# Optimization experiments

Measured on AMD Instinct MI355X. Metric: run time of the kernel, lower is better.

## Reference

```python
import jax, jax.numpy as jnp
import numpy as np

NEG_SLOPE = 0.2
LN_EPS = 1e-5


def setup_inputs() -> dict:
    key = jax.random.key(0)
    k1, k2, k3, k4 = jax.random.split(key, 4)
    B, K, D, H = 64, 256, 1024, 2
    x = jax.random.normal(k1, (B, K, D), dtype=jnp.float32)
    adj = jax.random.randint(k2, (K, K), 0, 2, dtype=jnp.int32)
    # Xavier-ish scaling for weights
    W = jax.random.normal(k3, (D, D), dtype=jnp.float32) * (1.0 / np.sqrt(D))
    a = jax.random.normal(k4, (H, 2 * D), dtype=jnp.float32) * (1.0 / np.sqrt(2 * D))
    gamma = jnp.ones((D,), dtype=jnp.float32)
    beta = jnp.zeros((D,), dtype=jnp.float32)
    return {"x": x, "adj": adj, "W": W, "a": a, "gamma": gamma, "beta": beta}


def _layer_norm(y, gamma, beta):
    mu = jnp.mean(y, axis=-1, keepdims=True)
    var = jnp.mean(jnp.square(y - mu), axis=-1, keepdims=True)
    return (y - mu) * jax.lax.rsqrt(var + LN_EPS) * gamma + beta


def reference(x, adj, W, a, gamma, beta):
    # x: (B,K,D), adj: (K,K), W: (D,D), a: (H,2D)
    D = W.shape[1]
    h = jnp.einsum("bki,io->bko", x, W)  # (B,K,D)
    # GAT trick: a^T [h_i; h_j] = a_src . h_i + a_dst . h_j (same math as
    # the huge pairwise-concat + Linear in the original module).
    a_src, a_dst = a[:, :D], a[:, D:]  # each (H,D)
    f_i = jnp.einsum("bkd,hd->bhk", h, a_src)  # (B,H,K)
    f_j = jnp.einsum("bkd,hd->bhk", h, a_dst)  # (B,H,K)
    e = f_i[:, :, :, None] + f_j[:, :, None, :]  # (B,H,K,K)
    e = jnp.where(e >= 0, e, NEG_SLOPE * e)  # LeakyReLU
    mask = (adj != 0)[None, None]  # (1,1,K,K)
    e = jnp.where(mask, e, -jnp.inf)
    attn = jax.nn.softmax(e, axis=-1)
    attn = jnp.where(jnp.isnan(attn), 0.0, attn)  # nan_to_num for all-masked rows
    # dropout is identity in eval mode
    head_out = jnp.einsum("bhij,bjd->bhid", attn, h)  # (B,H,K,D)
    out = jnp.mean(head_out, axis=1)  # average heads, (B,K,D)
    out = _layer_norm(out + x, gamma, beta)  # residual is Identity (in_dim==out_dim)
    return out
```

## Files before the change

### kernel.cpp

```cpp
#include <hip/hip_runtime.h>
#include <hip/hip_bf16.h>

#define KN 256
#define DD 1024
#define HH 2

typedef __attribute__((ext_vector_type(8))) short short8;
typedef __attribute__((ext_vector_type(4))) float f32x4;

__device__ __forceinline__ ushort f2b(float f) {
  union { float f; unsigned u; } v; v.f = f;
  unsigned u = v.u;
  return (ushort)((u + 0x7fffu + ((u >> 16) & 1u)) >> 16);
}
__device__ __forceinline__ float b2f(ushort h) {
  union { unsigned u; float f; } v; v.u = ((unsigned)h) << 16;
  return v.f;
}
__device__ __forceinline__ void gload16(const ushort* g, ushort* l) {
  __builtin_amdgcn_global_load_lds(
      (const __attribute__((address_space(1))) void*)g,
      (__attribute__((address_space(3))) void*)l, 16, 0, 0);
}

__global__ __launch_bounds__(256) void k_conv(const float* __restrict__ x,
                                              ushort* __restrict__ xb) {
  int c0 = blockIdx.x * 256 + threadIdx.x;
  for (int it = 0; it < 4; ++it) {
    size_t i = ((size_t)c0 + (size_t)it * 524288) * 8;
    float4 v0 = *reinterpret_cast<const float4*>(&x[i]);
    float4 v1 = *reinterpret_cast<const float4*>(&x[i + 4]);
    short8 o;
    o[0] = (short)f2b(v0.x); o[1] = (short)f2b(v0.y);
    o[2] = (short)f2b(v0.z); o[3] = (short)f2b(v0.w);
    o[4] = (short)f2b(v1.x); o[5] = (short)f2b(v1.y);
    o[6] = (short)f2b(v1.z); o[7] = (short)f2b(v1.w);
    *reinterpret_cast<short8*>(&xb[i]) = o;
  }
}

__global__ __launch_bounds__(256) void k_wT(const float* __restrict__ W, ushort* __restrict__ WTb) {
  __shared__ float t[32][33];
  int tx = threadIdx.x, ty = threadIdx.y;
  int x = blockIdx.x * 32 + tx;
  int y0 = blockIdx.y * 32 + ty;
  for (int i = 0; i < 32; i += 8)
    t[ty + i][tx] = W[(size_t)(y0 + i) * DD + x];
  __syncthreads();
  int xo = blockIdx.y * 32 + tx;
  int yo = blockIdx.x * 32 + ty;
  for (int i = 0; i < 32; i += 8)
    WTb[(size_t)(yo + i) * DD + xo] = f2b(t[tx][ty + i]);
}

__global__ __launch_bounds__(512, 2) void k_gemm_h(const ushort* __restrict__ xb,
                                                   const ushort* __restrict__ WTb,
                                                   ushort* __restrict__ hT) {
  __shared__ ushort As[2][16384];
  __shared__ ushort Bs[2][16384];
  const int tid = threadIdx.x;
  const int w = tid >> 6, lane = tid & 63;
  const int bn = blockIdx.x;
  const int b  = blockIdx.y;
  const int wm = (w >> 2) * 128, wn = (w & 3) * 64;
  const int r16 = lane & 15, kqi = lane >> 4;
  const ushort* gA0 = xb + (size_t)(b * 256) * DD;
  const ushort* gB0 = WTb + (size_t)(bn * 256) * DD;
  const int srow0 = tid >> 3;
  const int scc   = (tid & 7) ^ ((tid >> 3) & 7);
  const int sdst0 = (tid & ~63) * 8;
  const int cs0 = (kqi)     ^ (r16 & 7);
  const int cs1 = (kqi + 4) ^ (r16 & 7);
  f32x4 acc[8][4] = {};
  short8 bfv[4][2];

#define STG(ISB, BUF, H, KB)                                                    \
  {                                                                             \
    const ushort* g0_ = (ISB) ? gB0 : gA0;                                      \
    ushort* l0_ = (ISB) ? Bs[BUF] : As[BUF];                                    \
    gload16(g0_ + (size_t)((H) * 128 + srow0) * DD + (KB) + scc * 8,            \
            l0_ + (H) * 8192 + sdst0);                                          \
    gload16(g0_ + (size_t)((H) * 128 + 64 + srow0) * DD + (KB) + scc * 8,       \
            l0_ + (H) * 8192 + 4096 + sdst0);                                   \
  }

#define PHASE(Q, BUF, LOADB, WMODE, STAGE_STMT)                                 \
  {                                                                             \
    short8 af0[2], af1[2];                                                      \
    {                                                                           \
      const ushort* Ab_ = As[BUF];                                              \
      int ra_ = (wm + (Q) * 32 + r16) * 64;                                     \
      int rb_ = (wm + (Q) * 32 + 16 + r16) * 64;                                \
      af0[0] = *(const short8*)(Ab_ + ra_ + cs0 * 8);                           \
      af0[1] = *(const short8*)(Ab_ + ra_ + cs1 * 8);                           \
      af1[0] = *(const short8*)(Ab_ + rb_ + cs0 * 8);                           \
      af1[1] = *(const short8*)(Ab_ + rb_ + cs1 * 8);                           \
    }                                                                           \
    if (LOADB) {                                                                \
      const ushort* Bb_ = Bs[BUF];                                              \
      _Pragma("unroll")                                                         \
      for (int nf = 0; nf < 4; ++nf) {                                          \
        int rn_ = (wn + nf * 16 + r16) * 64;                                    \
        bfv[nf][0] = *(const short8*)(Bb_ + rn_ + cs0 * 8);                     \
        bfv[nf][1] = *(const short8*)(Bb_ + rn_ + cs1 * 8);                     \
      }                                                                         \
    }                                                                           \
    STAGE_STMT;                                                                 \
    __builtin_amdgcn_s_barrier();                                               \
    asm volatile("s_waitcnt lgkmcnt(0)" ::: "memory");                          \
    __builtin_amdgcn_sched_barrier(0);                                          \
    __builtin_amdgcn_s_setprio(1);                                              \
    _Pragma("unroll")                                                           \
    for (int nf = 0; nf < 4; ++nf) {                                            \
      acc[(Q)*2][nf]   = __builtin_amdgcn_mfma_f32_16x16x32_bf16(af0[0], bfv[nf][0], acc[(Q)*2][nf], 0, 0, 0);     \
      acc[(Q)*2+1][nf] = __builtin_amdgcn_mfma_f32_16x16x32_bf16(af1[0], bfv[nf][0], acc[(Q)*2+1][nf], 0, 0, 0);   \
    }                                                                           \
    _Pragma("unroll")                                                           \
    for (int nf = 0; nf < 4; ++nf) {                                            \
      acc[(Q)*2][nf]   = __builtin_amdgcn_mfma_f32_16x16x32_bf16(af0[1], bfv[nf][1], acc[(Q)*2][nf], 0, 0, 0);     \
      acc[(Q)*2+1][nf] = __builtin_amdgcn_mfma_f32_16x16x32_bf16(af1[1], bfv[nf][1], acc[(Q)*2+1][nf], 0, 0, 0);   \
    }                                                                           \
    __builtin_amdgcn_s_setprio(0);                                              \
    __builtin_amdgcn_sched_barrier(0);                                          \
    if ((WMODE) == 1) { asm volatile("s_waitcnt vmcnt(6)" ::: "memory"); }      \
    else if ((WMODE) == 2) { asm volatile("s_waitcnt vmcnt(0)" ::: "memory"); } \
    __builtin_amdgcn_s_barrier();                                               \
  }

  STG(1, 0, 0, 0) STG(1, 0, 1, 0) STG(0, 0, 0, 0) STG(0, 0, 1, 0)
  STG(1, 1, 0, 64) STG(1, 1, 1, 64) STG(0, 1, 0, 64)
  asm volatile("s_waitcnt vmcnt(6)" ::: "memory");
  __builtin_amdgcn_sched_barrier(0);
  __builtin_amdgcn_s_barrier();

  for (int i = 0; i < 8; ++i) {
    const int k1 = i * 128 + 64;
    const int k2 = i * 128 + 128;
    const int k3 = i * 128 + 192;
    const bool s2 = (k2 < 1024), s3 = (k3 < 1024);
    const int wt = (i < 7) ? 1 : 2;
    PHASE(0, 0, 1, 0,  { STG(0, 1, 1, k1) })
    PHASE(1, 0, 0, 0,  { if (s2) STG(1, 0, 0, k2) })
    PHASE(2, 0, 0, 0,  { if (s2) STG(1, 0, 1, k2) })
    PHASE(3, 0, 0, wt, { if (s2) STG(0, 0, 0, k2) })
    PHASE(0, 1, 1, 0,  { if (s2) STG(0, 0, 1, k2) })
    PHASE(1, 1, 0, 0,  { if (s3) STG(1, 1, 0, k3) })
    PHASE(2, 1, 0, 0,  { if (s3) STG(1, 1, 1, k3) })
    PHASE(3, 1, 0, wt, { if (s3) STG(0, 1, 0, k3) })
  }
#undef PHASE
#undef STG

  const int g = lane >> 4;
  #pragma unroll
  for (int mf = 0; mf < 8; ++mf) {
    int j0 = wm + mf * 16 + g * 4;
    #pragma unroll
    for (int nf = 0; nf < 4; ++nf) {
      int C = bn * 256 + wn + nf * 16 + r16;
      ushort4 o;
      o.x = f2b(acc[mf][nf][0]); o.y = f2b(acc[mf][nf][1]);
      o.z = f2b(acc[mf][nf][2]); o.w = f2b(acc[mf][nf][3]);
      *reinterpret_cast<ushort4*>(&hT[((size_t)b * DD + C) * KN + j0]) = o;
    }
  }
}

__global__ __launch_bounds__(256) void k_f(const ushort* __restrict__ hT,
                                           const float* __restrict__ a,
                                           float* __restrict__ fip, float* __restrict__ fjp) {
  __shared__ float als[4][256];
  int b = blockIdx.x, dq = blockIdx.y;
  int tid = threadIdx.x;
  for (int v = 0; v < 4; ++v) als[v][tid] = a[v * DD + dq * 256 + tid];
  __syncthreads();
  const ushort* base = hT + ((size_t)b * DD + dq * 256) * KN + tid;
  float a0 = 0.f, a1 = 0.f, a2 = 0.f, a3 = 0.f;
  #pragma unroll 8
  for (int d = 0; d < 256; ++d) {
    float hv = b2f(base[(size_t)d * KN]);
    a0 += hv * als[0][d];
    a1 += hv * als[1][d];
    a2 += hv * als[2][d];
    a3 += hv * als[3][d];
  }
  size_t o = ((size_t)(dq * 64 + b) * HH) * KN + tid;
  fip[o] = a0;
  fjp[o] = a1;
  fip[o + KN] = a2;
  fjp[o + KN] = a3;
}

__global__ __launch_bounds__(256) void k_attn(const float* __restrict__ fip, const float* __restrict__ fjp,
                                              const int* __restrict__ adj, ushort* __restrict__ Pb) {
  int w = threadIdx.x >> 6, l = threadIdx.x & 63;
  int gw = blockIdx.x * 4 + w;
  int b = gw >> 8, i = gw & 255;
  int4 am = *reinterpret_cast<const int4*>(adj + i * KN + l * 4);
  int msk[4] = { am.x, am.y, am.z, am.w };
  float fi0 = 0.f, fi1 = 0.f;
  float fj0[4] = {0.f, 0.f, 0.f, 0.f}, fj1[4] = {0.f, 0.f, 0.f, 0.f};
  for (int dq = 0; dq < 4; ++dq) {
    size_t o = ((size_t)(dq * 64 + b) * HH) * KN;
    fi0 += fip[o + i];
    fi1 += fip[o + KN + i];
    float4 t0 = *reinterpret_cast<const float4*>(&fjp[o + l * 4]);
    float4 t1 = *reinterpret_cast<const float4*>(&fjp[o + KN + l * 4]);
    fj0[0] += t0.x; fj0[1] += t0.y; fj0[2] += t0.z; fj0[3] += t0.w;
    fj1[0] += t1.x; fj1[1] += t1.y; fj1[2] += t1.z; fj1[3] += t1.w;
  }
  float e0[4], e1[4];
  const float NEGINF = -3.0e38f;
  float m0 = NEGINF, m1 = NEGINF;
  for (int e = 0; e < 4; ++e) {
    float v0 = fi0 + fj0[e], v1 = fi1 + fj1[e];
    v0 = v0 >= 0.f ? v0 : 0.2f * v0;
    v1 = v1 >= 0.f ? v1 : 0.2f * v1;
    e0[e] = v0; e1[e] = v1;
    if (msk[e]) { m0 = fmaxf(m0, v0); m1 = fmaxf(m1, v1); }
  }
  for (int off = 1; off < 64; off <<= 1) {
    m0 = fmaxf(m0, __shfl_xor(m0, off));
    m1 = fmaxf(m1, __shfl_xor(m1, off));
  }
  float p0[4], p1[4], s0 = 0.f, s1 = 0.f;
  for (int e = 0; e < 4; ++e) {
    p0[e] = msk[e] ? __expf(e0[e] - m0) : 0.f;
    p1[e] = msk[e] ? __expf(e1[e] - m1) : 0.f;
    s0 += p0[e]; s1 += p1[e];
  }
  for (int off = 1; off < 64; off <<= 1) {
    s0 += __shfl_xor(s0, off);
    s1 += __shfl_xor(s1, off);
  }
  float i0 = s0 > 0.f ? 1.f / s0 : 0.f;
  float i1 = s1 > 0.f ? 1.f / s1 : 0.f;
  ushort4 o;
  o.x = f2b(0.5f * (p0[0] * i0 + p1[0] * i1));
  o.y = f2b(0.5f * (p0[1] * i0 + p1[1] * i1));
  o.z = f2b(0.5f * (p0[2] * i0 + p1[2] * i1));
  o.w = f2b(0.5f * (p0[3] * i0 + p1[3] * i1));
  *reinterpret_cast<ushort4*>(&Pb[((size_t)b * KN + i) * KN + l * 4]) = o;
}

__global__ __launch_bounds__(512) void k_gemm_o(const ushort* __restrict__ Pb,
                                                const ushort* __restrict__ hT,
                                                ushort* __restrict__ yx,
                                                float* __restrict__ pstats) {
  __shared__ ushort As[2][8192];
  __shared__ ushort Bs[2][4096];
  __shared__ float red2[256][2][2];
  const int b = blockIdx.x;
  const int dt = blockIdx.y;
  const int tid = threadIdx.x;
  const int w = tid >> 6, lane = tid & 63;
  const int wm = (w >> 1) * 64;
  const int wn = (w & 1) * 64;
  const int r16 = lane & 15, kqi = lane >> 4;
  const ushort* PbB = Pb + (size_t)b * KN * KN;
  const ushort* hTB = hT + ((size_t)b * DD + dt * 128) * KN;
  f32x4 acc[4][4] = {};
  const int wb = tid & ~63;

  #define OSTAGE(buf, kt)                                                          \
    {                                                                              \
      _Pragma("unroll")                                                            \
      for (int s = 0; s < 2; ++s) {                                                \
        int slot = s * 512 + tid;                                                  \
        int row = slot >> 2, kc = slot & 3;                                        \
        gload16(PbB + (size_t)row * KN + (kt) + kc * 8,                            \
                As[buf] + (size_t)(s * 512 + wb) * 8);                             \
      }                                                                            \
      {                                                                            \
        int row = tid >> 2, kc = tid & 3;                                          \
        gload16(hTB + (size_t)row * KN + (kt) + kc * 8,                            \
                Bs[buf] + (size_t)wb * 8);                                         \
      }                                                                            \
    }

  OSTAGE(0, 0);
  OSTAGE(1, 32);
  for (int it8 = 0; it8 < 8; ++it8) {
    const int cur = it8 & 1;
    if (it8 < 7) asm volatile("s_waitcnt vmcnt(3)" ::: "memory");
    else         asm volatile("s_waitcnt vmcnt(0)" ::: "memory");
    __builtin_amdgcn_s_barrier();
    __builtin_amdgcn_sched_barrier(0);
    const ushort* Ac = As[cur];
    const ushort* Bc = Bs[cur];
    short8 af[4], bf[4];
    #pragma unroll
    for (int mf = 0; mf < 4; ++mf) {
      int row = wm + mf * 16 + r16;
      af[mf] = *reinterpret_cast<const short8*>(Ac + (size_t)row * 32 + kqi * 8);
    }
    #pragma unroll
    for (int nf = 0; nf < 4; ++nf) {
      int row = wn + nf * 16 + r16;
      bf[nf] = *reinterpret_cast<const short8*>(Bc + (size_t)row * 32 + kqi * 8);
    }
    #pragma unroll
    for (int mf = 0; mf < 4; ++mf)
      #pragma unroll
      for (int nf = 0; nf < 4; ++nf)
        acc[mf][nf] = __builtin_amdgcn_mfma_f32_16x16x32_bf16(af[mf], bf[nf], acc[mf][nf], 0, 0, 0);
    __builtin_amdgcn_sched_barrier(0);
    __builtin_amdgcn_s_barrier();
    if (it8 < 6)
      OSTAGE(cur, (it8 + 2) * 32);
  }
  #undef OSTAGE

  const int g = lane >> 4;
  float ps[4][4] = {}, qs[4][4] = {};
  #pragma unroll
  for (int mf = 0; mf < 4; ++mf)
    #pragma unroll
    for (int nf = 0; nf < 4; ++nf) {
      int C = dt * 128 + wn + nf * 16 + r16;
      #pragma unroll
      for (int rr = 0; rr < 4; ++rr) {
        int i = wm + mf * 16 + g * 4 + rr;
        size_t gi = ((size_t)(b * KN + i)) * DD + C;
        float v = acc[mf][nf][rr] + b2f(yx[gi]);
        yx[gi] = f2b(v);
        ps[mf][rr] += v; qs[mf][rr] += v * v;
      }
    }
  #pragma unroll
  for (int off = 1; off < 16; off <<= 1)
    #pragma unroll
    for (int mf = 0; mf < 4; ++mf)
      #pragma unroll
      for (int rr = 0; rr < 4; ++rr) {
        ps[mf][rr] += __shfl_xor(ps[mf][rr], off);
        qs[mf][rr] += __shfl_xor(qs[mf][rr], off);
      }
  if (r16 == 0) {
    #pragma unroll
    for (int mf = 0; mf < 4; ++mf)
      #pragma unroll
      for (int rr = 0; rr < 4; ++rr) {
        int i = wm + mf * 16 + g * 4 + rr;
        red2[i][w & 1][0] = ps[mf][rr];
        red2[i][w & 1][1] = qs[mf][rr];
      }
  }
  __syncthreads();
  if (tid < 256) {
    float S = red2[tid][0][0] + red2[tid][1][0];
    float Q = red2[tid][0][1] + red2[tid][1][1];
    size_t o = ((size_t)(dt * 64 + b) * KN + tid) * 2;
    pstats[o] = S;
    pstats[o + 1] = Q;
  }
}

__global__ __launch_bounds__(256) void k_ln(const ushort* __restrict__ y,
                                            const float* __restrict__ pstats,
                                            const float* __restrict__ gamma,
                                            const float* __restrict__ beta,
                                            float* __restrict__ out) {
  int tid = threadIdx.x;
  size_t row = blockIdx.x;
  int b = (int)(row >> 8), i = (int)(row & 255);
  float S = 0.f, Q = 0.f;
  #pragma unroll
  for (int dt = 0; dt < 8; ++dt) {
    size_t o = ((size_t)(dt * 64 + b) * KN + i) * 2;
    S += pstats[o];
    Q += pstats[o + 1];
  }
  float mu = S * (1.0f / DD);
  float var = Q * (1.0f / DD) - mu * mu;
  float inv = rsqrtf(var + 1e-5f);
  ushort4 v = *reinterpret_cast<const ushort4*>(&y[row * DD + tid * 4]);
  float4 gm = *reinterpret_cast<const float4*>(&gamma[tid * 4]);
  float4 bt = *reinterpret_cast<const float4*>(&beta[tid * 4]);
  float4 o;
  o.x = (b2f(v.x) - mu) * inv * gm.x + bt.x;
  o.y = (b2f(v.y) - mu) * inv * gm.y + bt.y;
  o.z = (b2f(v.z) - mu) * inv * gm.z + bt.z;
  o.w = (b2f(v.w) - mu) * inv * gm.w + bt.w;
  *reinterpret_cast<float4*>(&out[row * DD + tid * 4]) = o;
}

extern "C" void kernel_launch(void* const* d_in, const int* in_sizes, int n_in,
                              void* d_out, int out_size, void* d_ws, size_t ws_size,
                              hipStream_t stream) {
  const float* x     = (const float*)d_in[0];
  const int*   adj   = (const int*)d_in[1];
  const float* W     = (const float*)d_in[2];
  const float* a     = (const float*)d_in[3];
  const float* gamma = (const float*)d_in[4];
  const float* beta  = (const float*)d_in[5];
  float* out = (float*)d_out;

  char* ws = (char*)d_ws;
  const size_t OFS_WT = 0;
  const size_t OFS_XB = 2097152;
  const size_t OFS_HT = 35651584;
  const size_t OFS_PB = 69206016;
  const size_t NEED   = 77856768;
  if (ws_size < NEED) return;

  ushort* WTb   = (ushort*)(ws + OFS_WT);
  float*  fip   = (float*)(ws + OFS_WT);
  float*  fjp   = (float*)(ws + OFS_WT + 524288);
  float*  pst   = (float*)(ws + OFS_WT);
  ushort* xb    = (ushort*)(ws + OFS_XB);
  ushort* hT    = (ushort*)(ws + OFS_HT);
  ushort* Pb    = (ushort*)(ws + OFS_PB);

  k_conv<<<2048, 256, 0, stream>>>(x, xb);
  k_wT<<<dim3(32, 32), dim3(32, 8), 0, stream>>>(W, WTb);
  k_gemm_h<<<dim3(4, 64), 512, 0, stream>>>(xb, WTb, hT);
  k_f<<<dim3(64, 4), 256, 0, stream>>>(hT, a, fip, fjp);
  k_attn<<<4096, 256, 0, stream>>>(fip, fjp, adj, Pb);
  k_gemm_o<<<dim3(64, 8), 512, 0, stream>>>(Pb, hT, xb, pst);
  k_ln<<<16384, 256, 0, stream>>>(xb, pst, gamma, beta, out);
}
```

Before: 137.5 us.

## Fuse attention-score projections into GEMM epilogue and remap block grid

Computes the a_src/a_dst dot products directly from the fp32 GEMM accumulators in k_gemm_h's epilogue. It reduces them with lane shuffles and a small shared-memory buffer across warps, which removes the separate k_f kernel that re-read hT from global memory. The grid is flattened and remapped so neighbouring blocks share batch/column tiles, likely for L2 locality. WTb is moved to the Pb workspace region to avoid aliasing with fip/fjp, which are now written during the GEMM. The cost is extra epilogue work and added shared memory in the GEMM, which may lower occupancy.

```diff
diff --git a/kernel.cpp b/kernel.cpp
--- a/kernel.cpp
+++ b/kernel.cpp
@@ -55,13 +55,18 @@
 
 __global__ __launch_bounds__(512, 2) void k_gemm_h(const ushort* __restrict__ xb,
                                                    const ushort* __restrict__ WTb,
-                                                   ushort* __restrict__ hT) {
+                                                   const float* __restrict__ a,
+                                                   ushort* __restrict__ hT,
+                                                   float* __restrict__ fip,
+                                                   float* __restrict__ fjp) {
   __shared__ ushort As[2][16384];
   __shared__ ushort Bs[2][16384];
+  __shared__ float fls[4][256][4];
   const int tid = threadIdx.x;
   const int w = tid >> 6, lane = tid & 63;
-  const int bn = blockIdx.x;
-  const int b  = blockIdx.y;
+  const int flat = blockIdx.x;
+  const int bn = (flat >> 3) & 3;
+  const int b  = (flat & 7) + 8 * (flat >> 5);
   const int wm = (w >> 2) * 128, wn = (w & 3) * 64;
   const int r16 = lane & 15, kqi = lane >> 4;
   const ushort* gA0 = xb + (size_t)(b * 256) * DD;
@@ -164,31 +169,48 @@
       *reinterpret_cast<ushort4*>(&hT[((size_t)b * DD + C) * KN + j0]) = o;
     }
   }
-}
-
-__global__ __launch_bounds__(256) void k_f(const ushort* __restrict__ hT,
-                                           const float* __restrict__ a,
-                                           float* __restrict__ fip, float* __restrict__ fjp) {
-  __shared__ float als[4][256];
-  int b = blockIdx.x, dq = blockIdx.y;
-  int tid = threadIdx.x;
-  for (int v = 0; v < 4; ++v) als[v][tid] = a[v * DD + dq * 256 + tid];
+
+  float av[4][4];
+  #pragma unroll
+  for (int nf = 0; nf < 4; ++nf) {
+    int C = bn * 256 + wn + nf * 16 + r16;
+    av[nf][0] = a[C];
+    av[nf][1] = a[DD + C];
+    av[nf][2] = a[2 * DD + C];
+    av[nf][3] = a[3 * DD + C];
+  }
+  #pragma unroll
+  for (int mf = 0; mf < 8; ++mf)
+    #pragma unroll
+    for (int rr = 0; rr < 4; ++rr) {
+      float s0 = 0.f, s1 = 0.f, s2 = 0.f, s3 = 0.f;
+      #pragma unroll
+      for (int nf = 0; nf < 4; ++nf) {
+        float hv = acc[mf][nf][rr];
+        s0 += hv * av[nf][0]; s1 += hv * av[nf][1];
+        s2 += hv * av[nf][2]; s3 += hv * av[nf][3];
+      }
+      #pragma unroll
+      for (int off = 1; off < 16; off <<= 1) {
+        s0 += __shfl_xor(s0, off); s1 += __shfl_xor(s1, off);
+        s2 += __shfl_xor(s2, off); s3 += __shfl_xor(s3, off);
+      }
+      if (r16 == 0) {
+        int j = wm + mf * 16 + g * 4 + rr;
+        fls[w & 3][j][0] = s0; fls[w & 3][j][1] = s1;
+        fls[w & 3][j][2] = s2; fls[w & 3][j][3] = s3;
+      }
+    }
   __syncthreads();
-  const ushort* base = hT + ((size_t)b * DD + dq * 256) * KN + tid;
-  float a0 = 0.f, a1 = 0.f, a2 = 0.f, a3 = 0.f;
-  #pragma unroll 8
-  for (int d = 0; d < 256; ++d) {
-    float hv = b2f(base[(size_t)d * KN]);
-    a0 += hv * als[0][d];
-    a1 += hv * als[1][d];
-    a2 += hv * als[2][d];
-    a3 += hv * als[3][d];
-  }
-  size_t o = ((size_t)(dq * 64 + b) * HH) * KN + tid;
-  fip[o] = a0;
-  fjp[o] = a1;
-  fip[o + KN] = a2;
-  fjp[o + KN] = a3;
+  if (tid < 256) {
+    float v0 = fls[0][tid][0] + fls[1][tid][0] + fls[2][tid][0] + fls[3][tid][0];
+    float v1 = fls[0][tid][1] + fls[1][tid][1] + fls[2][tid][1] + fls[3][tid][1];
+    float v2 = fls[0][tid][2] + fls[1][tid][2] + fls[2][tid][2] + fls[3][tid][2];
+    float v3 = fls[0][tid][3] + fls[1][tid][3] + fls[2][tid][3] + fls[3][tid][3];
+    size_t o = ((size_t)(bn * 64 + b) * HH) * KN + tid;
+    fip[o] = v0; fjp[o] = v1;
+    fip[o + KN] = v2; fjp[o + KN] = v3;
+  }
 }
 
 __global__ __launch_bounds__(256) void k_attn(const float* __restrict__ fip, const float* __restrict__ fjp,
@@ -397,25 +419,24 @@
   float* out = (float*)d_out;
 
   char* ws = (char*)d_ws;
-  const size_t OFS_WT = 0;
+  const size_t OFS_FP = 0;
   const size_t OFS_XB = 2097152;
   const size_t OFS_HT = 35651584;
   const size_t OFS_PB = 69206016;
   const size_t NEED   = 77856768;
   if (ws_size < NEED) return;
 
-  ushort* WTb   = (ushort*)(ws + OFS_WT);
-  float*  fip   = (float*)(ws + OFS_WT);
-  float*  fjp   = (float*)(ws + OFS_WT + 524288);
-  float*  pst   = (float*)(ws + OFS_WT);
+  float*  fip   = (float*)(ws + OFS_FP);
+  float*  fjp   = (float*)(ws + OFS_FP + 524288);
+  float*  pst   = (float*)(ws + OFS_FP);
   ushort* xb    = (ushort*)(ws + OFS_XB);
   ushort* hT    = (ushort*)(ws + OFS_HT);
+  ushort* WTb   = (ushort*)(ws + OFS_PB);
   ushort* Pb    = (ushort*)(ws + OFS_PB);
 
   k_conv<<<2048, 256, 0, stream>>>(x, xb);
   k_wT<<<dim3(32, 32), dim3(32, 8), 0, stream>>>(W, WTb);
-  k_gemm_h<<<dim3(4, 64), 512, 0, stream>>>(xb, WTb, hT);
-  k_f<<<dim3(64, 4), 256, 0, stream>>>(hT, a, fip, fjp);
+  k_gemm_h<<<256, 512, 0, stream>>>(xb, WTb, a, hT, fip, fjp);
   k_attn<<<4096, 256, 0, stream>>>(fip, fjp, adj, Pb);
   k_gemm_o<<<dim3(64, 8), 512, 0, stream>>>(Pb, hT, xb, pst);
   k_ln<<<16384, 256, 0, stream>>>(xb, pst, gamma, beta, out);
```

Measured after the change: 132.3 us. 1.04x faster.
